# Optimization experiments

Hardware: AMD Instinct MI355X
Metric: run time of the kernel (lower is better)

Reference implementation:

```python
import jax, jax.numpy as jnp
import numpy as np

N = 100000      # nodes
D = 64          # raw node feature dim
E = 3200000     # edges
G = 128         # graphs in batch
RANK = 50
OVER = 10       # randomized-SVD oversampling
NPOW = 4        # subspace (power) iterations
ALPHA = 0.85    # pagerank alpha
HID = 32
NCLS = 696
F = 21 * D      # concat of [x] + 4 hop-1 + 16 hop-2 propagated tensors


def setup_inputs() -> dict:
    key = jax.random.key(0)
    ks = jax.random.split(key, 8)
    x = jax.random.normal(ks[0], (N, D), jnp.float32)
    rows = jax.random.randint(ks[1], (E,), 0, N, jnp.int32)
    cols = jax.random.randint(ks[2], (E,), 0, N, jnp.int32)
    graph_ids = jnp.sort(jax.random.randint(ks[3], (N,), 0, G, jnp.int32))
    w = jax.random.normal(ks[4], (F, 64), jnp.float32) / np.float32(np.sqrt(F))
    W1 = jax.random.normal(ks[5], (64, HID), jnp.float32) / np.float32(8.0)
    b1 = jnp.zeros((HID,), jnp.float32)
    W2 = jax.random.normal(ks[6], (HID, NCLS), jnp.float32) / np.float32(np.sqrt(HID))
    return dict(x=x, rows=rows, cols=cols, graph_ids=graph_ids, num_graphs=G,
                w=w, W1=W1, b1=b1, W2=W2)


def _prop_ops(X, rows, cols, deg, n):
    """Apply the 4 sparse operators to X. A[r,c]=1 per edge (rows[k], cols[k])."""
    ax = jax.ops.segment_sum(X[cols], rows, num_segments=n)          # A @ X
    t = ax / jnp.where(deg > 0, deg, 1.0)[:, None]                   # D^{-1} A @ X (transition)
    pr = ALPHA * t + ((1.0 - ALPHA) / n) * ax                        # pagerank-style operator
    dw = ax / (deg + 1e-5)[:, None]                                  # deepwalk: diag(1/(deg+eps)) A
    return [ax, t, pr, dw]


def _propagated(x, rows, cols):
    n = x.shape[0]
    deg = jax.ops.segment_sum(jnp.ones(rows.shape, x.dtype), rows, num_segments=n)
    h1 = _prop_ops(x, rows, cols, deg, n)                            # 4 tensors, hop 1
    h2 = [t2 for t1 in h1 for t2 in _prop_ops(t1, rows, cols, deg, n)]  # 16 tensors, hop 2
    return jnp.concatenate([x] + h1 + h2, axis=-1)                   # [n, 21*D]


def _rsvd(h, rank, key):
    """Deterministic randomized SVD (Halko et al.), QR-stabilized power iterations."""
    k = rank + OVER
    omega = jax.random.normal(key, (h.shape[1], k), h.dtype)
    Q = jnp.linalg.qr(h @ omega)[0]                                  # [n, k]
    for _ in range(NPOW):
        Q = jnp.linalg.qr(h.T @ Q)[0]
        Q = jnp.linalg.qr(h @ Q)[0]
    B = Q.T @ h                                                      # [k, F]
    ub, s, vt = jnp.linalg.svd(B, full_matrices=False)
    return (Q @ ub)[:, :rank], s[:rank], vt[:rank]


def reference(x, rows, cols, graph_ids, num_graphs, w, W1, b1, W2):
    h = _propagated(x, rows, cols)                                   # [n, F]
    u, s, vt = _rsvd(h, RANK, jax.random.key(42))
    us = u * s                                                       # [n, rank]
    term = us @ (vt @ w)                                             # [n, 64]
    hid = jax.nn.leaky_relu(term @ W1 + b1)                          # Dense + leaky_relu
    out_nodes = hid @ W2                                             # [n, num_classes]
    # pooling_adj.T.normalize_right(): each node belongs to exactly one graph,
    # so the column sums are 1 and this is a per-graph segment sum.
    return jax.ops.segment_sum(out_nodes, graph_ids, num_segments=num_graphs)
```

## Files before the change

### kernel.cpp

```cpp
#include <hip/hip_runtime.h>

#define NN   100000
#define DD   64
#define EE   3200000
#define GG   128
#define FF   1344
#define KK   60
#define RK   50
#define HIDN 32
#define NCL  696
#define BSPLIT 96
#define GSL  64
#define PN   40


typedef short short8 __attribute__((ext_vector_type(8)));
typedef float f32x4 __attribute__((ext_vector_type(4)));

__device__ __forceinline__ unsigned short f2bf(float x){
  unsigned u = __float_as_uint(x);
  unsigned r = u + 0x7fffu + ((u>>16)&1u);
  return (unsigned short)(r>>16);
}
__device__ __forceinline__ float bf2f(unsigned short h){
  return __uint_as_float(((unsigned)h)<<16);
}

__device__ __forceinline__ unsigned rotl32(unsigned x, unsigned r){ return (x<<r)|(x>>(32u-r)); }

__device__ __forceinline__ void threefry(unsigned& x0, unsigned& x1){
  const unsigned ks0 = 0u, ks1 = 42u, ks2 = 0x1BD11BDAu ^ 0u ^ 42u;
  unsigned ks[3] = {ks0, ks1, ks2};
  const unsigned rotA[4] = {13u,15u,26u,6u};
  const unsigned rotB[4] = {17u,29u,16u,24u};
  x0 += ks0; x1 += ks1;
  #pragma unroll
  for (int i = 0; i < 5; ++i){
    #pragma unroll
    for (int j = 0; j < 4; ++j){
      unsigned r = (i & 1) ? rotB[j] : rotA[j];
      x0 += x1; x1 = rotl32(x1, r); x1 ^= x0;
    }
    x0 += ks[(i+1)%3]; x1 += ks[(i+2)%3] + (unsigned)(i+1);
  }
}

__device__ __forceinline__ float bits_to_normal(unsigned bits){
  unsigned mant = bits >> 9;
  float f; { unsigned fb = 0x3f800000u | mant; f = __uint_as_float(fb); }
  f -= 1.0f;
  const float lo = -0.99999994f;
  float u = fmaf(f, 2.0f, lo);
  u = fmaxf(lo, u);
  float w = -log1pf(-u*u);
  float p;
  if (w < 5.0f){
    w -= 2.5f;
    p = 2.81022636e-08f;
    p = fmaf(p, w, 3.43273939e-07f);
    p = fmaf(p, w, -3.5233877e-06f);
    p = fmaf(p, w, -4.39150654e-06f);
    p = fmaf(p, w, 0.00021858087f);
    p = fmaf(p, w, -0.00125372503f);
    p = fmaf(p, w, -0.00417768164f);
    p = fmaf(p, w, 0.246640727f);
    p = fmaf(p, w, 1.50140941f);
  } else {
    w = sqrtf(w) - 3.0f;
    p = -0.000200214257f;
    p = fmaf(p, w, 0.000100950558f);
    p = fmaf(p, w, 0.00134934322f);
    p = fmaf(p, w, -0.00367342844f);
    p = fmaf(p, w, 0.00573950773f);
    p = fmaf(p, w, -0.0076224613f);
    p = fmaf(p, w, 0.00943887047f);
    p = fmaf(p, w, 1.00167406f);
    p = fmaf(p, w, 2.83297682f);
  }
  return 1.41421356f * (p * u);
}

__global__ void k_omega(float* __restrict__ om){
  int i = blockIdx.x*blockDim.x + threadIdx.x;
  if (i >= FF*KK) return;
  unsigned x0 = 0u, x1 = (unsigned)i;
  threefry(x0, x1);
  om[i] = bits_to_normal(x0 ^ x1);
}

__global__ void k_count(const int* __restrict__ rows, int* __restrict__ cnt){
  int e = blockIdx.x*blockDim.x + threadIdx.x;
  if (e < EE) atomicAdd(&cnt[rows[e]], 1);
}

__global__ __launch_bounds__(1024) void k_scan1(const int* __restrict__ cnt,
    int* __restrict__ incl, int* __restrict__ bsums){
  __shared__ int buf[1024];
  int i = blockIdx.x*1024 + threadIdx.x;
  int v = (i < NN) ? cnt[i] : 0;
  buf[threadIdx.x] = v; __syncthreads();
  for (int ofs = 1; ofs < 1024; ofs <<= 1){
    int add = (threadIdx.x >= (unsigned)ofs) ? buf[threadIdx.x - ofs] : 0;
    __syncthreads();
    buf[threadIdx.x] += add;
    __syncthreads();
  }
  if (i < NN) incl[i] = buf[threadIdx.x];
  if (threadIdx.x == 1023) bsums[blockIdx.x] = buf[1023];
}

__global__ void k_scan2(int* __restrict__ bsums, int nb){
  if (threadIdx.x == 0){
    int run = 0;
    for (int i = 0; i < nb; ++i){ int v = bsums[i]; bsums[i] = run; run += v; }
  }
}

__global__ void k_scan3(const int* __restrict__ cnt, const int* __restrict__ bsums,
                        int* __restrict__ rowptr){
  int i = blockIdx.x*blockDim.x + threadIdx.x;
  if (i >= NN) return;
  int incl = rowptr[i];
  int ex = incl - cnt[i] + bsums[i >> 10];
  rowptr[i] = ex;
  if (i == NN-1) rowptr[NN] = ex + cnt[i];
}

__global__ void k_scatter(const int* __restrict__ rows, const int* __restrict__ cols,
                          const int* __restrict__ rowptr, int* __restrict__ tmpc,
                          int* __restrict__ csr){
  int e = blockIdx.x*blockDim.x + threadIdx.x;
  if (e >= EE) return;
  int r = rows[e];
  int p = atomicAdd(&tmpc[r], 1);
  csr[rowptr[r] + p] = cols[e];
}

__global__ void k_degr(const int* __restrict__ cnt, float* __restrict__ r1, float* __restrict__ r2){
  int i = blockIdx.x*blockDim.x + threadIdx.x;
  if (i >= NN) return;
  int d = cnt[i];
  float fd = (float)d;
  r1[i] = (d > 0) ? 1.0f/fd : 1.0f;
  r2[i] = 1.0f/(fd + 1e-5f);
}

__global__ void k_xcvt(const float* __restrict__ x,
                       unsigned short* __restrict__ xh, unsigned short* __restrict__ xl){
  int gid = blockIdx.x*blockDim.x + threadIdx.x;
  if (gid >= NN*64) return;
  float v = x[gid];
  unsigned short h = f2bf(v);
  xh[gid] = h;
  xl[gid] = f2bf(v - bf2f(h));
}

__global__ __launch_bounds__(256) void k_hop1(const float* __restrict__ x,
    const int* __restrict__ rp, const int* __restrict__ cc, float* __restrict__ ax,
    unsigned short* __restrict__ axh, unsigned short* __restrict__ axl){
  int n = blockIdx.x*4 + (threadIdx.x >> 6);
  int lane = threadIdx.x & 63;
  if (n >= NN) return;
  int s = rp[n], e = rp[n+1];
  float acc = 0.f;
  int idx = s;
  for (; idx + 8 <= e; idx += 8){
    int c0 = cc[idx], c1 = cc[idx+1], c2 = cc[idx+2], c3 = cc[idx+3];
    int c4 = cc[idx+4], c5 = cc[idx+5], c6 = cc[idx+6], c7 = cc[idx+7];
    float v0 = x[(size_t)c0*64 + lane];
    float v1 = x[(size_t)c1*64 + lane];
    float v2 = x[(size_t)c2*64 + lane];
    float v3 = x[(size_t)c3*64 + lane];
    float v4 = x[(size_t)c4*64 + lane];
    float v5 = x[(size_t)c5*64 + lane];
    float v6 = x[(size_t)c6*64 + lane];
    float v7 = x[(size_t)c7*64 + lane];
    acc += ((v0 + v1) + (v2 + v3)) + ((v4 + v5) + (v6 + v7));
  }
  for (; idx < e; ++idx) acc += x[(size_t)cc[idx]*64 + lane];
  size_t o = (size_t)n*64 + lane;
  ax[o] = acc;
  unsigned short h = f2bf(acc);
  axh[o] = h;
  axl[o] = f2bf(acc - bf2f(h));
}

__global__ __launch_bounds__(256) void k_hop2(const int* __restrict__ rp, const int* __restrict__ cc,
    const float* __restrict__ ax, const float* __restrict__ r1, const float* __restrict__ r2,
    unsigned short* __restrict__ s0h, unsigned short* __restrict__ s0l,
    unsigned short* __restrict__ s1h, unsigned short* __restrict__ s1l,
    unsigned short* __restrict__ s3h, unsigned short* __restrict__ s3l){
  int n = blockIdx.x*4 + (threadIdx.x >> 6);
  int lane = threadIdx.x & 63;
  if (n >= NN) return;
  int s = rp[n], e = rp[n+1];
  float v_s0 = 0.f, v_s1 = 0.f, v_s3 = 0.f;
  int idx = s;
  for (; idx + 8 <= e; idx += 8){
    int c0 = cc[idx], c1 = cc[idx+1], c2 = cc[idx+2], c3 = cc[idx+3];
    int c4 = cc[idx+4], c5 = cc[idx+5], c6 = cc[idx+6], c7 = cc[idx+7];
    float v0 = ax[(size_t)c0*64 + lane], a0 = r1[c0], b0 = r2[c0];
    float v1 = ax[(size_t)c1*64 + lane], a1 = r1[c1], b1 = r2[c1];
    float v2 = ax[(size_t)c2*64 + lane], a2 = r1[c2], b2 = r2[c2];
    float v3 = ax[(size_t)c3*64 + lane], a3 = r1[c3], b3 = r2[c3];
    float v4 = ax[(size_t)c4*64 + lane], a4 = r1[c4], b4 = r2[c4];
    float v5 = ax[(size_t)c5*64 + lane], a5 = r1[c5], b5 = r2[c5];
    float v6 = ax[(size_t)c6*64 + lane], a6 = r1[c6], b6 = r2[c6];
    float v7 = ax[(size_t)c7*64 + lane], a7 = r1[c7], b7 = r2[c7];
    v_s0 += ((v0 + v1) + (v2 + v3)) + ((v4 + v5) + (v6 + v7));
    v_s1 = fmaf(v0,a0,fmaf(v1,a1,fmaf(v2,a2,fmaf(v3,a3,v_s1))));
    v_s1 = fmaf(v4,a4,fmaf(v5,a5,fmaf(v6,a6,fmaf(v7,a7,v_s1))));
    v_s3 = fmaf(v0,b0,fmaf(v1,b1,fmaf(v2,b2,fmaf(v3,b3,v_s3))));
    v_s3 = fmaf(v4,b4,fmaf(v5,b5,fmaf(v6,b6,fmaf(v7,b7,v_s3))));
  }
  for (; idx < e; ++idx){
    int c = cc[idx];
    float v = ax[(size_t)c*64 + lane];
    v_s0 += v;
    v_s1 = fmaf(v, r1[c], v_s1);
    v_s3 = fmaf(v, r2[c], v_s3);
  }
  size_t o = (size_t)n*64 + lane;
  unsigned short h0 = f2bf(v_s0);
  s0h[o] = h0; s0l[o] = f2bf(v_s0 - bf2f(h0));
  unsigned short h1 = f2bf(v_s1);
  s1h[o] = h1; s1l[o] = f2bf(v_s1 - bf2f(h1));
  unsigned short h3 = f2bf(v_s3);
  s3h[o] = h3; s3l[o] = f2bf(v_s3 - bf2f(h3));
}

__global__ void k_beff(const float* __restrict__ B,
                       unsigned short* __restrict__ Beh, unsigned short* __restrict__ Bel){
  int gid = blockIdx.x*blockDim.x + threadIdx.x;
  if (gid >= 20*4096) return;
  int p = gid >> 12;
  int rem = gid & 4095;
  int c = rem >> 6, r = rem & 63;
  int t = p >> 2, j = p & 3;
  float val = 0.f;
  if (c < KK){
    if (t == 0)      val = (j == 0) ? B[(0*64 + r)*60 + c] : 0.f;
    else if (t == 1) val = B[((1+j)*64 + r)*60 + c];
    else if (t == 2) val = B[((5+j)*64 + r)*60 + c] + 1.5e-6f*B[((13+j)*64 + r)*60 + c];
    else if (t == 3) val = B[((9+j)*64 + r)*60 + c] + 0.85f  *B[((13+j)*64 + r)*60 + c];
    else             val = B[((17+j)*64 + r)*60 + c];
  }
  unsigned short h = f2bf(val);
  Beh[gid] = h;
  Bel[gid] = f2bf(val - bf2f(h));
}

__global__ __launch_bounds__(256) void k_beffT(const float* __restrict__ Z,
    const float* __restrict__ Rtot,
    unsigned short* __restrict__ Beh, unsigned short* __restrict__ Bel){
  __shared__ float Br[64][61];
  __shared__ float Rt[60][64];
  int p = blockIdx.x;
  int t2 = p >> 2, j = p & 3;
  int tid = threadIdx.x;
  if (t2 == 0 && j != 0){
    for (int o = tid; o < 4096; o += 256){ Beh[(size_t)p*4096 + o] = 0; Bel[(size_t)p*4096 + o] = 0; }
    return;
  }
  for (int i = tid; i < 3840; i += 256){
    int r = i >> 6, c = i & 63;
    if (c < 60) Rt[r][c] = Rtot[r*60 + c];
  }
  for (int o = tid; o < 64*60; o += 256){
    int r = o / 60, k = o - (o/60)*60;
    float v;
    if (t2 == 0)      v = Z[(0*64 + r)*60 + k];
    else if (t2 == 1) v = Z[((1+j)*64 + r)*60 + k];
    else if (t2 == 2) v = Z[((5+j)*64 + r)*60 + k] + 1.5e-6f*Z[((13+j)*64 + r)*60 + k];
    else if (t2 == 3) v = Z[((9+j)*64 + r)*60 + k] + 0.85f  *Z[((13+j)*64 + r)*60 + k];
    else              v = Z[((17+j)*64 + r)*60 + k];
    Br[r][k] = v;
  }
  __syncthreads();
  for (int o = tid; o < 4096; o += 256){
    int c = o >> 6, r = o & 63;
    float s = 0.f;
    if (c < KK){
      #pragma unroll 10
      for (int kp = 0; kp < 60; ++kp) s = fmaf(Br[r][kp], Rt[kp][c], s);
    }
    unsigned short h = f2bf(s);
    Beh[(size_t)p*4096 + o] = h;
    Bel[(size_t)p*4096 + o] = f2bf(s - bf2f(h));
  }
}

__global__ __launch_bounds__(256) void k_qcvt(const float* __restrict__ Q,
    const float* __restrict__ r1, const float* __restrict__ r2,
    unsigned short* __restrict__ Qjh, unsigned short* __restrict__ Qjl){
  __shared__ float Qs[64][65];
  __shared__ float c1s[64], c3s[64];
  int n0 = blockIdx.x*64;
  int tid = threadIdx.x;
  for (int i = tid; i < 64*60; i += 256){
    int nl = i/60, k = i - (i/60)*60;
    int gn = n0 + nl;
    Qs[nl][k] = (gn < NN) ? Q[(size_t)gn*KK + k] : 0.f;
  }
  if (tid < 64){
    int gn = n0 + tid;
    c1s[tid] = (gn < NN) ? r1[gn] : 0.f;
    c3s[tid] = (gn < NN) ? r2[gn] : 0.f;
  }
  __syncthreads();
  for (int o = tid; o < 3*64*64; o += 256){
    int nl = o & 63;
    int jk = o >> 6;
    int gn = n0 + nl;
    if (gn >= NN) continue;
    int j = jk >> 6, k = jk & 63;
    float v = (k < KK) ? Qs[nl][k] : 0.f;
    float c = (j == 0) ? 1.f : ((j == 1) ? c1s[nl] : c3s[nl]);
    float sv = c * v;
    unsigned short h = f2bf(sv);
    Qjh[(size_t)jk*NN + gn] = h;
    Qjl[(size_t)jk*NN + gn] = f2bf(sv - bf2f(h));
  }
}

__device__ __forceinline__ void fma44(const float4 a, const float4 b, float (&acc)[4][4]){
  acc[0][0] = fmaf(a.x,b.x,acc[0][0]); acc[0][1] = fmaf(a.x,b.y,acc[0][1]);
  acc[0][2] = fmaf(a.x,b.z,acc[0][2]); acc[0][3] = fmaf(a.x,b.w,acc[0][3]);
  acc[1][0] = fmaf(a.y,b.x,acc[1][0]); acc[1][1] = fmaf(a.y,b.y,acc[1][1]);
  acc[1][2] = fmaf(a.y,b.z,acc[1][2]); acc[1][3] = fmaf(a.y,b.w,acc[1][3]);
  acc[2][0] = fmaf(a.z,b.x,acc[2][0]); acc[2][1] = fmaf(a.z,b.y,acc[2][1]);
  acc[2][2] = fmaf(a.z,b.z,acc[2][2]); acc[2][3] = fmaf(a.z,b.w,acc[2][3]);
  acc[3][0] = fmaf(a.w,b.x,acc[3][0]); acc[3][1] = fmaf(a.w,b.y,acc[3][1]);
  acc[3][2] = fmaf(a.w,b.z,acc[3][2]); acc[3][3] = fmaf(a.w,b.w,acc[3][3]);
}

__global__ __launch_bounds__(256) void k_fwd(
    const unsigned short* __restrict__ xh, const unsigned short* __restrict__ xl,
    const unsigned short* __restrict__ axh, const unsigned short* __restrict__ axl,
    const unsigned short* __restrict__ s0h, const unsigned short* __restrict__ s0l,
    const unsigned short* __restrict__ s1h, const unsigned short* __restrict__ s1l,
    const unsigned short* __restrict__ s3h, const unsigned short* __restrict__ s3l,
    const unsigned short* __restrict__ Beh, const unsigned short* __restrict__ Bel,
    const float* __restrict__ r1, const float* __restrict__ r2,
    float* __restrict__ Y, float* __restrict__ Cpart){
  __shared__ __align__(16) unsigned short AB[4*64*72];
  __shared__ float cS[4][64];
  unsigned short* Ah = AB;
  unsigned short* Al = AB + 64*72;
  unsigned short* Bh = AB + 2*64*72;
  unsigned short* Bl = AB + 3*64*72;
  float* As2 = (float*)AB;
  const unsigned short* Tsh[5] = {xh, axh, s0h, s1h, s3h};
  const unsigned short* Tsl[5] = {xl, axl, s0l, s1l, s3l};
  int n0 = blockIdx.x*64;
  int tid = threadIdx.x;
  int lane = tid & 63, wid = tid >> 6;
  int rowb = (wid & 1)*32, colb = (wid >> 1)*32;
  int l15 = lane & 15, l4 = lane >> 4;

  if (tid < 64){
    int gn = n0 + tid;
    float r1v = 0.f, r2v = 0.f, one = 0.f;
    if (gn < NN){ r1v = r1[gn]; r2v = r2[gn]; one = 1.f; }
    cS[0][tid] = one;
    cS[1][tid] = r1v;
    cS[2][tid] = fmaf(0.85f, r1v, 1.5e-6f*one);
    cS[3][tid] = r2v;
  }

  f32x4 master[2][2] = {};
  int curt = -1;
  for (int plin = 0; plin < 17; ++plin){
    int t  = (plin == 0) ? 0 : (((plin-1) >> 2) + 1);
    int jj = (plin == 0) ? 0 : ((plin-1) & 3);
    int p  = (plin == 0) ? 0 : (plin + 3);
    if (t != curt){
      __syncthreads();
      const unsigned short* Th = Tsh[t];
      const unsigned short* Tl = Tsl[t];
      #pragma unroll
      for (int l = 0; l < 2; ++l){
        int li = tid + l*256;
        int n = li >> 3, f8 = (li & 7)*8;
        int gn = n0 + n;
        uint4 hv = make_uint4(0,0,0,0), lv = make_uint4(0,0,0,0);
        if (gn < NN){
          hv = *(const uint4*)(Th + (size_t)gn*64 + f8);
          lv = *(const uint4*)(Tl + (size_t)gn*64 + f8);
        }
        *(uint4*)(Ah + n*72 + f8) = hv;
        *(uint4*)(Al + n*72 + f8) = lv;
      }
      curt = t;
    }
    __syncthreads();
    #pragma unroll
    for (int l = 0; l < 2; ++l){
      int li = tid + l*256;
      int c = li >> 3, k8 = (li & 7)*8;
      uint4 hv = *(const uint4*)(Beh + (size_t)p*4096 + c*64 + k8);
      uint4 lv = *(const uint4*)(Bel + (size_t)p*4096 + c*64 + k8);
      *(uint4*)(Bh + c*72 + k8) = hv;
      *(uint4*)(Bl + c*72 + k8) = lv;
    }
    __syncthreads();

    float cvv[2][4];
    #pragma unroll
    for (int rg = 0; rg < 2; ++rg)
      #pragma unroll
      for (int r = 0; r < 4; ++r)
        cvv[rg][r] = cS[jj][rowb + rg*16 + l4*4 + r];

    f32x4 part[2][2] = {};
    #pragma unroll
    for (int s = 0; s < 2; ++s){
      int kc = s*32 + l4*8;
      short8 a0h = *(const short8*)(Ah + (rowb      + l15)*72 + kc);
      short8 a1h = *(const short8*)(Ah + (rowb + 16 + l15)*72 + kc);
      short8 a0l = *(const short8*)(Al + (rowb      + l15)*72 + kc);
      short8 a1l = *(const short8*)(Al + (rowb + 16 + l15)*72 + kc);
      #pragma unroll
      for (int cg = 0; cg < 2; ++cg){
        short8 bh = *(const short8*)(Bh + (colb + cg*16 + l15)*72 + kc);
        short8 bl = *(const short8*)(Bl + (colb + cg*16 + l15)*72 + kc);
        part[0][cg] = __builtin_amdgcn_mfma_f32_16x16x32_bf16(a0h, bh, part[0][cg], 0, 0, 0);
        part[0][cg] = __builtin_amdgcn_mfma_f32_16x16x32_bf16(a0h, bl, part[0][cg], 0, 0, 0);
        part[0][cg] = __builtin_amdgcn_mfma_f32_16x16x32_bf16(a0l, bh, part[0][cg], 0, 0, 0);
        part[1][cg] = __builtin_amdgcn_mfma_f32_16x16x32_bf16(a1h, bh, part[1][cg], 0, 0, 0);
        part[1][cg] = __builtin_amdgcn_mfma_f32_16x16x32_bf16(a1h, bl, part[1][cg], 0, 0, 0);
        part[1][cg] = __builtin_amdgcn_mfma_f32_16x16x32_bf16(a1l, bh, part[1][cg], 0, 0, 0);
      }
    }
    #pragma unroll
    for (int rg = 0; rg < 2; ++rg)
      #pragma unroll
      for (int cg = 0; cg < 2; ++cg)
        #pragma unroll
        for (int r = 0; r < 4; ++r)
          master[rg][cg][r] = fmaf(cvv[rg][r], part[rg][cg][r], master[rg][cg][r]);
  }

  #pragma unroll
  for (int rg = 0; rg < 2; ++rg)
    #pragma unroll
    for (int cg = 0; cg < 2; ++cg)
      #pragma unroll
      for (int r = 0; r < 4; ++r){
        int n = rowb + rg*16 + l4*4 + r;
        int c = colb + cg*16 + l15;
        int gn = n0 + n;
        if (gn < NN && c < KK) Y[(size_t)gn*KK + c] = master[rg][cg][r];
      }

  __syncthreads();
  #pragma unroll
  for (int rg = 0; rg < 2; ++rg)
    #pragma unroll
    for (int cg = 0; cg < 2; ++cg)
      #pragma unroll
      for (int r = 0; r < 4; ++r){
        int n = rowb + rg*16 + l4*4 + r;
        int c = colb + cg*16 + l15;
        As2[n*68 + c] = master[rg][cg][r];
      }
  __syncthreads();
  {
    int tx = tid & 15, ty = tid >> 4;
    float g[4][4] = {};
    #pragma unroll 4
    for (int n = 0; n < 64; ++n){
      float4 a = *(const float4*)(As2 + n*68 + tx*4);
      float4 b = *(const float4*)(As2 + n*68 + ty*4);
      fma44(a, b, g);
    }
    float* slab = Cpart + (size_t)(blockIdx.x & (GSL-1))*3600;
    #pragma unroll
    for (int i = 0; i < 4; ++i){
      int r = tx*4 + i;
      #pragma unroll
      for (int j = 0; j < 4; ++j){
        int c = ty*4 + j;
        if (r < KK && c < KK) atomicAdd(&slab[r*KK + c], g[i][j]);
      }
    }
  }
}

__global__ __launch_bounds__(256) void k_bwd(
    const unsigned short* __restrict__ xh, const unsigned short* __restrict__ xl,
    const unsigned short* __restrict__ axh, const unsigned short* __restrict__ axl,
    const unsigned short* __restrict__ s0h, const unsigned short* __restrict__ s0l,
    const unsigned short* __restrict__ s1h, const unsigned short* __restrict__ s1l,
    const unsigned short* __restrict__ s3h, const unsigned short* __restrict__ s3l,
    const unsigned short* __restrict__ Qjh, const unsigned short* __restrict__ Qjl,
    float* __restrict__ Ppart){
  const unsigned short* Th = (blockIdx.x==0)?xh:(blockIdx.x==1)?axh:(blockIdx.x==2)?s0h:(blockIdx.x==3)?s1h:s3h;
  const unsigned short* Tl = (blockIdx.x==0)?xl:(blockIdx.x==1)?axl:(blockIdx.x==2)?s0l:(blockIdx.x==3)?s1l:s3l;
  const int TT = (NN + 31)/32;
  int per = (TT + BSPLIT - 1)/BSPLIT;
  int t0 = blockIdx.y * per;
  int t1 = t0 + per; if (t1 > TT) t1 = TT;

  __shared__ __align__(16) unsigned short Ah[64*PN];
  __shared__ __align__(16) unsigned short Al[64*PN];
  __shared__ __align__(16) unsigned short Bh3[3*64*PN];
  __shared__ __align__(16) unsigned short Bl3[3*64*PN];

  int tid = threadIdx.x;
  int lane = tid & 63, wid = tid >> 6;
  int rowb = (wid & 1)*32, colb = (wid >> 1)*32;
  int l15 = lane & 15, l4 = lane >> 4;

  f32x4 master[3][2][2] = {};

  for (int tl = t0; tl < t1; ++tl){
    int nb = tl*32;
    __syncthreads();
    {
      int n = tid >> 3, f8 = (tid & 7)*8;
      int gn = nb + n;
      uint4 hv = make_uint4(0,0,0,0), lv = make_uint4(0,0,0,0);
      if (gn < NN){
        hv = *(const uint4*)(Th + (size_t)gn*64 + f8);
        lv = *(const uint4*)(Tl + (size_t)gn*64 + f8);
      }
      const unsigned short* hp = (const unsigned short*)&hv;
      const unsigned short* lp = (const unsigned short*)&lv;
      #pragma unroll
      for (int i = 0; i < 8; ++i){
        Ah[(f8+i)*PN + n] = hp[i];
        Al[(f8+i)*PN + n] = lp[i];
      }
    }
    #pragma unroll
    for (int u = 0; u < 3; ++u){
      int l = tid + u*256;
      int row = l >> 2, ch = (l & 3)*8;
      uint4 hv = *(const uint4*)(Qjh + (size_t)row*NN + nb + ch);
      uint4 lv = *(const uint4*)(Qjl + (size_t)row*NN + nb + ch);
      *(uint4*)(Bh3 + row*PN + ch) = hv;
      *(uint4*)(Bl3 + row*PN + ch) = lv;
    }
    __syncthreads();
    short8 a0h = *(const short8*)(Ah + (rowb      + l15)*PN + l4*8);
    short8 a1h = *(const short8*)(Ah + (rowb + 16 + l15)*PN + l4*8);
    short8 a0l = *(const short8*)(Al + (rowb      + l15)*PN + l4*8);
    short8 a1l = *(const short8*)(Al + (rowb + 16 + l15)*PN + l4*8);
    #pragma unroll
    for (int jj = 0; jj < 3; ++jj){
      #pragma unroll
      for (int cg = 0; cg < 2; ++cg){
        short8 bh = *(const short8*)(Bh3 + jj*64*PN + (colb + cg*16 + l15)*PN + l4*8);
        short8 bl = *(const short8*)(Bl3 + jj*64*PN + (colb + cg*16 + l15)*PN + l4*8);
        master[jj][0][cg] = __builtin_amdgcn_mfma_f32_16x16x32_bf16(a0h, bh, master[jj][0][cg], 0, 0, 0);
        master[jj][0][cg] = __builtin_amdgcn_mfma_f32_16x16x32_bf16(a0h, bl, master[jj][0][cg], 0, 0, 0);
        master[jj][0][cg] = __builtin_amdgcn_mfma_f32_16x16x32_bf16(a0l, bh, master[jj][0][cg], 0, 0, 0);
        master[jj][1][cg] = __builtin_amdgcn_mfma_f32_16x16x32_bf16(a1h, bh, master[jj][1][cg], 0, 0, 0);
        master[jj][1][cg] = __builtin_amdgcn_mfma_f32_16x16x32_bf16(a1h, bl, master[jj][1][cg], 0, 0, 0);
        master[jj][1][cg] = __builtin_amdgcn_mfma_f32_16x16x32_bf16(a1l, bh, master[jj][1][cg], 0, 0, 0);
      }
    }
  }

  float* dst = Ppart + (size_t)blockIdx.y * 76800;
  #pragma unroll
  for (int jj = 0; jj < 3; ++jj){
    int j = (jj == 2) ? 3 : jj;
    #pragma unroll
    for (int rg = 0; rg < 2; ++rg)
      #pragma unroll
      for (int cg = 0; cg < 2; ++cg)
        #pragma unroll
        for (int r = 0; r < 4; ++r){
          int f = rowb + rg*16 + l4*4 + r;
          int kcol = colb + cg*16 + l15;
          if (kcol < KK)
            dst[(size_t)((blockIdx.x*4 + j)*64 + f)*60 + kcol] = master[jj][rg][cg][r];
        }
  }
}

__global__ void k_zasm(const float* __restrict__ Ppart, float* __restrict__ Z){
  int gid = blockIdx.x*blockDim.x + threadIdx.x;
  if (gid >= FF*KK) return;
  int f = gid / 60, k = gid - (gid/60)*60;
  int b = f >> 6, fi = f & 63;
  auto raw = [&](int t, int j)->float{
    size_t e = (size_t)((t*4 + j)*64 + fi)*60 + k;
    float s = 0.f;
    for (int bb = 0; bb < BSPLIT; ++bb) s += Ppart[(size_t)bb*76800 + e];
    return s;
  };
  auto fetch = [&](int t, int j)->float{
    if (j == 2) return 0.85f*raw(t,1) + 1.5e-6f*raw(t,0);
    return raw(t,j);
  };
  float val;
  if (b == 0)      val = raw(0,0);
  else if (b < 5)  val = fetch(1, b-1);
  else if (b < 9)  val = fetch(2, b-5);
  else if (b < 13) val = fetch(3, b-9);
  else if (b < 17) val = 0.85f*fetch(3, b-13) + 1.5e-6f*fetch(2, b-13);
  else             val = fetch(4, b-17);
  Z[gid] = val;
}

__global__ __launch_bounds__(256) void k_syrkp(const float* __restrict__ X, int nrows,
                                               float* __restrict__ Cpart){
  const int TTs = (nrows + 15)/16;
  int per = (TTs + gridDim.x - 1)/gridDim.x;
  int t0 = blockIdx.x*per;
  int t1 = t0 + per; if (t1 > TTs) t1 = TTs;
  __shared__ float Xs[16][64];
  int tid = threadIdx.x;
  int tx = tid & 15, ty = tid >> 4;
  float acc[4][4] = {};
  for (int tl = t0; tl < t1; ++tl){
    int nbase = tl*16;
    if (tid < 240){
      int n = tid / 15, ci = tid - (tid/15)*15;
      float4 v = make_float4(0.f,0.f,0.f,0.f);
      int gn = nbase + n;
      if (gn < nrows) v = *(const float4*)(X + (size_t)gn*KK + ci*4);
      *(float4*)&Xs[n][ci*4] = v;
    } else {
      int n = tid - 240;
      Xs[n][60]=0.f; Xs[n][61]=0.f; Xs[n][62]=0.f; Xs[n][63]=0.f;
    }
    __syncthreads();
    #pragma unroll
    for (int n = 0; n < 16; ++n){
      float4 a = *(const float4*)&Xs[n][tx*4];
      float4 b = *(const float4*)&Xs[n][ty*4];
      fma44(a, b, acc);
    }
    __syncthreads();
  }
  float* dst = Cpart + (size_t)blockIdx.x*3600;
  #pragma unroll
  for (int i = 0; i < 4; ++i){
    int r = tx*4 + i;
    #pragma unroll
    for (int j = 0; j < 4; ++j){
      int c = ty*4 + j;
      if (r < KK && c < KK) dst[r*KK + c] = acc[i][j];
    }
  }
}

__global__ void k_cred(const float* __restrict__ Cpart, int nparts, float* __restrict__ Cm){
  int gid = blockIdx.x*blockDim.x + threadIdx.x;
  if (gid >= 3600) return;
  float s = 0.f;
  for (int b = 0; b < nparts; ++b) s += Cpart[(size_t)b*3600 + gid];
  Cm[gid] = s;
}

__global__ __launch_bounds__(256) void k_cholinv(const float* __restrict__ Cin,
                                                 float* __restrict__ Rinv){
  __shared__ float R[60][65];
  __shared__ float Ri[60][65];
  __shared__ float Tmp[30][33];
  __shared__ float ridge;
  int t = threadIdx.x;
  for (int i = t; i < 3840; i += 256){
    int r = i >> 6, c = i & 63;
    if (c < 60) R[r][c] = Cin[r*60 + c];
  }
  __syncthreads();
  if (t == 0){
    float tr = 0.f;
    for (int i = 0; i < 60; ++i) tr += R[i][i];
    ridge = 1e-7f*(tr/60.f) + 1e-30f;
  }
  __syncthreads();
  if (t < 60) R[t][t] += ridge;
  __syncthreads();
  for (int j = 0; j < 60; ++j){
    float d  = fmaxf(R[j][j], 1e-30f);
    float dp = (j > 0) ? fmaxf(R[j-1][j-1], 1e-30f) : 1.f;
    float inv = 1.0f / d;
    float rsp = (j > 0) ? (1.0f / sqrtf(dp)) : 1.f;
    int nrow = 59 - j;
    for (int task = t; task < (nrow+1)*64; task += 256){
      int rr = task >> 6, i2 = task & 63;
      if (rr < nrow){
        int k = j + 1 + rr;
        if (i2 >= k && i2 < 60) R[k][i2] -= R[j][k]*R[j][i2]*inv;
      } else {
        if (j > 0 && i2 >= j-1 && i2 < 60) R[j-1][i2] *= rsp;
      }
    }
    __syncthreads();
  }
  if (t == 0) R[59][59] = sqrtf(fmaxf(R[59][59], 1e-30f));
  __syncthreads();
  for (int i = t; i < 3840; i += 256){ int r = i >> 6, c = i & 63; Ri[r][c] = 0.f; }
  __syncthreads();
  if (t < 60){
    int c = t;
    int lo = (c < 30) ? 0 : 30;
    Ri[c][c] = 1.0f / R[c][c];
    for (int i = c-1; i >= lo; --i){
      float s = 0.f;
      for (int k = i+1; k <= c; ++k) s += R[i][k]*Ri[k][c];
      Ri[i][c] = -s / R[i][i];
    }
  }
  __syncthreads();
  for (int idx2 = t; idx2 < 960; idx2 += 256){
    int r = idx2 >> 5, c = idx2 & 31;
    if (c < 30){
      float s = 0.f;
      for (int k = 0; k <= c; ++k) s += R[r][30+k]*Ri[30+k][30+c];
      Tmp[r][c] = s;
    }
  }
  __syncthreads();
  for (int idx2 = t; idx2 < 960; idx2 += 256){
    int r = idx2 >> 5, c = idx2 & 31;
    if (c < 30){
      float s = 0.f;
      for (int k = r; k < 30; ++k) s += Ri[r][k]*Tmp[k][c];
      Ri[r][30+c] = -s;
    }
  }
  __syncthreads();
  for (int i = t; i < 3600; i += 256) Rinv[i] = Ri[i/60][i%60];
}

__global__ __launch_bounds__(256) void k_cholinv2(const float* __restrict__ Gin,
                                                  float* __restrict__ Rinv){
  __shared__ float G[60][65];
  __shared__ float RN[60][65];
  __shared__ float T1[60][65];
  __shared__ float G2[60][65];
  __shared__ float Tmp[30][33];
  __shared__ float ridge;
  int t = threadIdx.x;
  for (int i = t; i < 3840; i += 256){
    int r = i >> 6, c = i & 63;
    if (c < 60){ G[r][c] = Gin[r*60 + c]; RN[r][c] = Rinv[r*60 + c]; }
  }
  __syncthreads();
  for (int o = t; o < 3600; o += 256){
    int i = o/60, j = o - (o/60)*60;
    float s = 0.f;
    for (int k = 0; k <= j; ++k) s = fmaf(G[i][k], RN[k][j], s);
    T1[i][j] = s;
  }
  __syncthreads();
  for (int o = t; o < 3600; o += 256){
    int i = o/60, j = o - (o/60)*60;
    float s = 0.f;
    for (int k = 0; k <= i; ++k) s = fmaf(RN[k][i], T1[k][j], s);
    G2[i][j] = s;
  }
  __syncthreads();
  if (t == 0){
    float tr = 0.f;
    for (int i = 0; i < 60; ++i) tr += G2[i][i];
    ridge = 1e-7f*(tr/60.f) + 1e-30f;
  }
  __syncthreads();
  if (t < 60) G2[t][t] += ridge;
  __syncthreads();
  for (int j = 0; j < 60; ++j){
    float d  = fmaxf(G2[j][j], 1e-30f);
    float dp = (j > 0) ? fmaxf(G2[j-1][j-1], 1e-30f) : 1.f;
    float inv = 1.0f / d;
    float rsp = (j > 0) ? (1.0f / sqrtf(dp)) : 1.f;
    int nrow = 59 - j;
    for (int task = t; task < (nrow+1)*64; task += 256){
      int rr = task >> 6, i2 = task & 63;
      if (rr < nrow){
        int k = j + 1 + rr;
        if (i2 >= k && i2 < 60) G2[k][i2] -= G2[j][k]*G2[j][i2]*inv;
      } else {
        if (j > 0 && i2 >= j-1 && i2 < 60) G2[j-1][i2] *= rsp;
      }
    }
    __syncthreads();
  }
  if (t == 0) G2[59][59] = sqrtf(fmaxf(G2[59][59], 1e-30f));
  __syncthreads();
  for (int i = t; i < 3840; i += 256){ int r = i >> 6, c = i & 63; T1[r][c] = 0.f; }
  __syncthreads();
  if (t < 60){
    int c = t;
    int lo = (c < 30) ? 0 : 30;
    T1[c][c] = 1.0f / G2[c][c];
    for (int i = c-1; i >= lo; --i){
      float s = 0.f;
      for (int k = i+1; k <= c; ++k) s += G2[i][k]*T1[k][c];
      T1[i][c] = -s / G2[i][i];
    }
  }
  __syncthreads();
  for (int idx2 = t; idx2 < 960; idx2 += 256){
    int r = idx2 >> 5, c = idx2 & 31;
    if (c < 30){
      float s = 0.f;
      for (int k = 0; k <= c; ++k) s += G2[r][30+k]*T1[30+k][30+c];
      Tmp[r][c] = s;
    }
  }
  __syncthreads();
  for (int idx2 = t; idx2 < 960; idx2 += 256){
    int r = idx2 >> 5, c = idx2 & 31;
    if (c < 30){
      float s = 0.f;
      for (int k = r; k < 30; ++k) s += T1[r][k]*Tmp[k][c];
      T1[r][30+c] = -s;
    }
  }
  __syncthreads();
  for (int o = t; o < 3600; o += 256){
    int i = o/60, j = o - (o/60)*60;
    float s = 0.f;
    if (i <= j){
      for (int k = i; k <= j; ++k) s = fmaf(RN[i][k], T1[k][j], s);
    }
    Rinv[o] = s;
  }
}

__global__ __launch_bounds__(256) void k_applyR(const float* Yin,
    const float* __restrict__ Rinv, float* Xout, int nrows){
  __shared__ float Rs[3600];
  for (int i = threadIdx.x; i < 3600; i += 256) Rs[i] = Rinv[i];
  __syncthreads();
  int w = threadIdx.x >> 6, lane = threadIdx.x & 63;
  #pragma unroll
  for (int r = 0; r < 4; ++r){
    int n = blockIdx.x*16 + w*4 + r;
    if (n >= nrows) continue;
    const float* y = Yin + (size_t)n*KK;
    float accv = 0.f;
    #pragma unroll 10
    for (int k2 = 0; k2 < KK; ++k2) accv = fmaf(y[k2], Rs[k2*KK + lane], accv);
    if (lane < KK) Xout[(size_t)n*KK + lane] = accv;
  }
}

__global__ void k_wb(const float* __restrict__ Z, const float* __restrict__ w,
                     float* __restrict__ WB){
  int gid = blockIdx.x*blockDim.x + threadIdx.x;
  if (gid >= KK*64) return;
  int r = gid >> 6, d = gid & 63;
  float acc = 0.f;
  for (int f = 0; f < FF; ++f) acc = fmaf(Z[(size_t)f*KK + r], w[(size_t)f*64 + d], acc);
  WB[gid] = acc;
}

__global__ __launch_bounds__(512) void k_jacobi(const float* __restrict__ Min,
                                                float* __restrict__ U50){
  __shared__ float A[60][65];
  __shared__ float Vv[60][65];
  __shared__ float cs[32], sn[32];
  __shared__ int pp[32], qq[32];
  __shared__ float ev[64];
  __shared__ int idx[64];
  int t = threadIdx.x;
  for (int i = t; i < 3840; i += 512){
    int r = i >> 6, c = i & 63;
    if (c < 60){ A[r][c] = Min[r*60 + c]; Vv[r][c] = (r == c) ? 1.f : 0.f; }
  }
  __syncthreads();
  for (int sweep = 0; sweep < 3; ++sweep){
    for (int round = 0; round < 59; ++round){
      if (t < 30){
        int i = t, j2 = 59 - t;
        int p = (i == 0) ? 0 : ((i - 1 + round) % 59 + 1);
        int q = ((j2 - 1 + round) % 59 + 1);
        if (p > q){ int tv = p; p = q; q = tv; }
        pp[t] = p; qq[t] = q;
        float app = A[p][p], aqq = A[q][q], apq = A[p][q];
        float c, s;
        if (fabsf(apq) < 1e-36f){ c = 1.f; s = 0.f; }
        else {
          float tau = (aqq - app) / (2.f * apq);
          float tt = ((tau >= 0.f) ? 1.f : -1.f) / (fabsf(tau) + sqrtf(1.f + tau*tau));
          c = 1.f / sqrtf(1.f + tt*tt);
          s = tt * c;
        }
        cs[t] = c; sn[t] = s;
      }
      __syncthreads();
      for (int task = t; task < 1920; task += 512){
        int k = task >> 6, i = task & 63;
        if (i < 60){
          int p = pp[k], q = qq[k];
          float c = cs[k], s = sn[k];
          float aip = A[i][p], aiq = A[i][q];
          A[i][p] = c*aip - s*aiq;  A[i][q] = s*aip + c*aiq;
          float vip = Vv[i][p], viq = Vv[i][q];
          Vv[i][p] = c*vip - s*viq; Vv[i][q] = s*vip + c*viq;
        }
      }
      __syncthreads();
      for (int task = t; task < 1920; task += 512){
        int k = task >> 6, i = task & 63;
        if (i < 60){
          int p = pp[k], q = qq[k];
          float c = cs[k], s = sn[k];
          float api = A[p][i], aqi = A[q][i];
          A[p][i] = c*api - s*aqi;  A[q][i] = s*api + c*aqi;
        }
      }
      __syncthreads();
    }
  }
  if (t < 60) ev[t] = A[t][t];
  __syncthreads();
  if (t < 60){
    float mine = ev[t];
    int rank = 0;
    for (int j = 0; j < 60; ++j){
      float o = ev[j];
      if (o > mine || (o == mine && j < t)) ++rank;
    }
    if (rank < RK) idx[rank] = t;
  }
  __syncthreads();
  for (int i2 = t; i2 < 60*RK; i2 += 512){
    int r = i2 / RK, c = i2 - (i2/RK)*RK;
    U50[i2] = Vv[r][idx[c]];
  }
}

__global__ __launch_bounds__(256) void k_chain(const float* __restrict__ U50,
    const float* __restrict__ WB, const float* __restrict__ W1, float* __restrict__ TW1){
  __shared__ float Us[60][52];
  __shared__ float WBs[60][64];
  __shared__ float G[50][64];
  __shared__ float Ts[60][64];
  int t = threadIdx.x;
  for (int i = t; i < 60*RK; i += 256) Us[i/RK][i%RK] = U50[i];
  for (int i = t; i < 3840; i += 256) WBs[i>>6][i&63] = WB[i];
  __syncthreads();
  for (int o = t; o < RK*64; o += 256){
    int r = o >> 6, d = o & 63;
    float acc = 0.f;
    #pragma unroll 10
    for (int i = 0; i < KK; ++i) acc = fmaf(Us[i][r], WBs[i][d], acc);
    G[r][d] = acc;
  }
  __syncthreads();
  for (int o = t; o < KK*64; o += 256){
    int i = o >> 6, d = o & 63;
    float acc = 0.f;
    #pragma unroll 10
    for (int r = 0; r < RK; ++r) acc = fmaf(Us[i][r], G[r][d], acc);
    Ts[i][d] = acc;
  }
  __syncthreads();
  for (int o = t; o < KK*HIDN; o += 256){
    int i = o >> 5, j = o & 31;
    float acc = 0.f;
    #pragma unroll 8
    for (int d = 0; d < 64; ++d) acc = fmaf(Ts[i][d], W1[d*HIDN + j], acc);
    TW1[o] = acc;
  }
}

__global__ __launch_bounds__(256) void k_hid(const float* __restrict__ Q,
    const float* __restrict__ TW1, const float* __restrict__ b1, float* __restrict__ hid){
  __shared__ float Ts[KK*HIDN];
  __shared__ float bs[HIDN];
  for (int i = threadIdx.x; i < KK*HIDN; i += 256) Ts[i] = TW1[i];
  if (threadIdx.x < HIDN) bs[threadIdx.x] = b1[threadIdx.x];
  __syncthreads();
  int gid = blockIdx.x*256 + threadIdx.x;
  if (gid >= NN*HIDN) return;
  int n = gid >> 5, j = gid & 31;
  const float* q = Q + (size_t)n*KK;
  float a = bs[j];
  #pragma unroll 10
  for (int k2 = 0; k2 < KK; ++k2) a = fmaf(q[k2], Ts[k2*HIDN + j], a);
  hid[gid] = (a >= 0.f) ? a : 0.01f*a;
}

__global__ void k_gstart(const int* __restrict__ gids, int* __restrict__ gst){
  int g = blockIdx.x*blockDim.x + threadIdx.x;
  if (g > GG) return;
  if (g == GG){ gst[GG] = NN; return; }
  int lo = 0, hi = NN;
  while (lo < hi){ int mid = (lo + hi) >> 1; if (gids[mid] < g) lo = mid + 1; else hi = mid; }
  gst[g] = lo;
}

__global__ __launch_bounds__(256) void k_gpool(const float* __restrict__ hid,
    const int* __restrict__ gst, float* __restrict__ pooled){
  int g = blockIdx.x;
  __shared__ float part[8][32];
  int w = threadIdx.x >> 5, lane = threadIdx.x & 31;
  int s = gst[g], e = gst[g+1];
  float acc = 0.f;
  for (int n = s + w; n < e; n += 8)
    acc += hid[(size_t)n*HIDN + lane];
  part[w][lane] = acc;
  __syncthreads();
  if (w == 0){
    float v = 0.f;
    #pragma unroll
    for (int i = 0; i < 8; ++i) v += part[i][lane];
    pooled[g*HIDN + lane] = v;
  }
}

__global__ void k_out(const float* __restrict__ pooled, const float* __restrict__ W2,
                      float* __restrict__ out){
  int gid = blockIdx.x*blockDim.x + threadIdx.x;
  if (gid >= GG*NCL) return;
  int g = gid / NCL, c = gid - (gid/NCL)*NCL;
  const float* p = pooled + g*HIDN;
  float acc = 0.f;
  #pragma unroll
  for (int k = 0; k < HIDN; ++k) acc = fmaf(p[k], W2[(size_t)k*NCL + c], acc);
  out[gid] = acc;
}

extern "C" void kernel_launch(void* const* d_in, const int* in_sizes, int n_in,
                              void* d_out, int out_size, void* d_ws, size_t ws_size,
                              hipStream_t stream){
  (void)in_sizes; (void)n_in; (void)out_size;
  const float* x   = (const float*)d_in[0];
  const int*  rows = (const int*)d_in[1];
  const int*  cols = (const int*)d_in[2];
  const int*  gids = (const int*)d_in[3];
  const float* wM  = (const float*)d_in[5];
  const float* W1  = (const float*)d_in[6];
  const float* b1  = (const float*)d_in[7];
  const float* W2  = (const float*)d_in[8];
  float* out = (float*)d_out;

  char* base = (char*)d_ws;
  size_t off = 0;
  auto alloc = [&](size_t bytes)->char*{
    off = (off + 255) & ~(size_t)255;
    char* p = base + off; off += bytes; return p;
  };
  float* ax    = (float*)alloc((size_t)NN*64*4);
  int*   csr   = (int*)  alloc((size_t)EE*4);
  unsigned short* Qjh = (unsigned short*)ax;
  unsigned short* xh  = (unsigned short*)alloc((size_t)NN*64*2);
  unsigned short* xl  = (unsigned short*)alloc((size_t)NN*64*2);
  unsigned short* axh = (unsigned short*)alloc((size_t)NN*64*2);
  unsigned short* axl = (unsigned short*)alloc((size_t)NN*64*2);
  unsigned short* s0h = (unsigned short*)alloc((size_t)NN*64*2);
  unsigned short* s0l = (unsigned short*)alloc((size_t)NN*64*2);
  unsigned short* s1h = (unsigned short*)alloc((size_t)NN*64*2);
  unsigned short* s1l = (unsigned short*)alloc((size_t)NN*64*2);
  unsigned short* s3h = (unsigned short*)alloc((size_t)NN*64*2);
  unsigned short* s3l = (unsigned short*)alloc((size_t)NN*64*2);
  float* Y     = (float*)alloc((size_t)NN*KK*4);
  unsigned short* Qjl = (unsigned short*)alloc((size_t)3*64*NN*2);
  float* Ppart = (float*)alloc((size_t)BSPLIT*76800*4);
  unsigned short* Beh = (unsigned short*)alloc((size_t)20*4096*2);
  unsigned short* Bel = (unsigned short*)alloc((size_t)20*4096*2);
  float* Om    = (float*)alloc((size_t)FF*KK*4);
  float* Zf    = (float*)alloc((size_t)FF*KK*4);
  float* Cm    = (float*)alloc(3600*4);
  float* Rinv  = (float*)alloc(3600*4);
  float* Mm    = (float*)alloc(3600*4);
  float* U50   = (float*)alloc(60*RK*4);
  float* WB    = (float*)alloc(KK*64*4);
  float* TW1   = (float*)alloc(KK*HIDN*4);
  float* pooled= (float*)alloc((size_t)GG*HIDN*4);
  float* r1    = (float*)alloc((size_t)NN*4);
  float* r2    = (float*)alloc((size_t)NN*4);
  int* cnt     = (int*)alloc((size_t)NN*4);
  int* rowptr  = (int*)alloc((size_t)(NN+1)*4);
  int* tmpc    = (int*)alloc((size_t)NN*4);
  int* gst     = (int*)alloc((size_t)(GG+1)*4);
  int* bsums   = (int*)alloc(256*4);
  float* hid   = (float*)Qjl;
  float* Cpart = Ppart;
  if (off > ws_size) return;

  const int SCAN_B = (NN + 1023) / 1024;

  hipMemsetAsync(cnt, 0, (size_t)NN*4, stream);
  k_count<<<(EE+255)/256, 256, 0, stream>>>(rows, cnt);
  k_scan1<<<SCAN_B, 1024, 0, stream>>>(cnt, rowptr, bsums);
  k_scan2<<<1, 64, 0, stream>>>(bsums, SCAN_B);
  k_scan3<<<(NN+255)/256, 256, 0, stream>>>(cnt, bsums, rowptr);
  hipMemsetAsync(tmpc, 0, (size_t)NN*4, stream);
  k_scatter<<<(EE+255)/256, 256, 0, stream>>>(rows, cols, rowptr, tmpc, csr);
  k_degr<<<(NN+255)/256, 256, 0, stream>>>(cnt, r1, r2);

  k_xcvt<<<(NN*64+255)/256, 256, 0, stream>>>(x, xh, xl);
  k_hop1<<<(NN+3)/4, 256, 0, stream>>>(x, rowptr, csr, ax, axh, axl);
  k_hop2<<<(NN+3)/4, 256, 0, stream>>>(rowptr, csr, ax, r1, r2, s0h, s0l, s1h, s1l, s3h, s3l);

  k_omega<<<(FF*KK+255)/256, 256, 0, stream>>>(Om);

  auto fwdg = [&](){
    hipMemsetAsync(Cpart, 0, (size_t)GSL*3600*4, stream);
    k_fwd<<<(NN+63)/64, 256, 0, stream>>>(xh, xl, axh, axl, s0h, s0l, s1h, s1l, s3h, s3l,
                                          Beh, Bel, r1, r2, Y, Cpart);
  };
  auto bwd = [&](const float* Qbuf){
    k_qcvt<<<(NN+63)/64, 256, 0, stream>>>(Qbuf, r1, r2, Qjh, Qjl);
    k_bwd<<<dim3(5, BSPLIT), 256, 0, stream>>>(xh, xl, axh, axl, s0h, s0l, s1h, s1l, s3h, s3l,
                                               Qjh, Qjl, Ppart);
    k_zasm<<<(FF*KK+255)/256, 256, 0, stream>>>(Ppart, Zf);
  };

  k_beff<<<(20*4096+255)/256, 256, 0, stream>>>(Om, Beh, Bel);
  fwdg();

  for (int it = 0; it < 4; ++it){
    k_cred<<<15, 256, 0, stream>>>(Cpart, GSL, Cm);
    k_cholinv<<<1, 256, 0, stream>>>(Cm, Rinv);
    bwd(Y);
    k_syrkp<<<84, 256, 0, stream>>>(Zf, FF, Cpart);
    k_cred<<<15, 256, 0, stream>>>(Cpart, 84, Cm);
    k_cholinv2<<<1, 256, 0, stream>>>(Cm, Rinv);
    k_beffT<<<20, 256, 0, stream>>>(Zf, Rinv, Beh, Bel);
    fwdg();
  }

  k_cred<<<15, 256, 0, stream>>>(Cpart, GSL, Cm);
  k_cholinv<<<1, 256, 0, stream>>>(Cm, Rinv);
  k_applyR<<<(NN+15)/16, 256, 0, stream>>>(Y, Rinv, Y, NN);

  bwd(Y);
  k_syrkp<<<84, 256, 0, stream>>>(Zf, FF, Cpart);
  k_cred<<<15, 256, 0, stream>>>(Cpart, 84, Mm);
  k_wb<<<(KK*64+255)/256, 256, 0, stream>>>(Zf, wM, WB);

  k_jacobi<<<1, 512, 0, stream>>>(Mm, U50);
  k_chain<<<1, 256, 0, stream>>>(U50, WB, W1, TW1);

  k_hid<<<(NN*HIDN+255)/256, 256, 0, stream>>>(Y, TW1, b1, hid);
  k_gstart<<<1, 256, 0, stream>>>(gids, gst);
  k_gpool<<<GG, 256, 0, stream>>>(hid, gst, pooled);
  k_out<<<(GG*NCL+255)/256, 256, 0, stream>>>(pooled, W2, out);
}
```

Measured before the change: 4.033 ms.

## Pre-transpose propagated tensors for backward GEMM and fold final R into small matrices

Adds a one-time transpose kernel that writes the five bf16 hi/lo propagated tensors in feature-major layout, so the backward h^T Q GEMM can load A tiles with contiguous vector loads instead of scattered shared-memory transposes on every call. It also stops applying the final R^-1 to the full N×60 Y matrix. R^-1 is applied to the small F×60 Zf instead, and folded into the TW1 chain matrix. This saves a full pass over Y but needs extra workspace for the transposed copies, with a fallback path when that workspace is not available.

Measured after the change: 3.975 ms. About the same (-1.4%).

```diff
diff --git a/kernel.cpp b/kernel.cpp
--- a/kernel.cpp
+++ b/kernel.cpp
@@ -229,6 +229,49 @@
   s3h[o] = h3; s3l[o] = f2bf(v_s3 - bf2f(h3));
 }
 
+__global__ __launch_bounds__(256) void k_tcvt(
+    const unsigned short* __restrict__ xh, const unsigned short* __restrict__ xl,
+    const unsigned short* __restrict__ axh, const unsigned short* __restrict__ axl,
+    const unsigned short* __restrict__ s0h, const unsigned short* __restrict__ s0l,
+    const unsigned short* __restrict__ s1h, const unsigned short* __restrict__ s1l,
+    const unsigned short* __restrict__ s3h, const unsigned short* __restrict__ s3l,
+    unsigned short* __restrict__ TTh, unsigned short* __restrict__ TTl){
+  __shared__ unsigned short Sh[64][72];
+  __shared__ unsigned short Sl[64][72];
+  int t = blockIdx.y;
+  const unsigned short* inh = (t==0)?xh:(t==1)?axh:(t==2)?s0h:(t==3)?s1h:s3h;
+  const unsigned short* inl = (t==0)?xl:(t==1)?axl:(t==2)?s0l:(t==3)?s1l:s3l;
+  int n0 = blockIdx.x*64;
+  int tid = threadIdx.x;
+  #pragma unroll
+  for (int l = 0; l < 2; ++l){
+    int li = tid + l*256;
+    int n = li >> 3, f8 = (li & 7)*8;
+    int gn = n0 + n;
+    uint4 hv = make_uint4(0,0,0,0), lv = make_uint4(0,0,0,0);
+    if (gn < NN){
+      hv = *(const uint4*)(inh + (size_t)gn*64 + f8);
+      lv = *(const uint4*)(inl + (size_t)gn*64 + f8);
+    }
+    *(uint4*)(&Sh[n][f8]) = hv;
+    *(uint4*)(&Sl[n][f8]) = lv;
+  }
+  __syncthreads();
+  #pragma unroll
+  for (int l = 0; l < 2; ++l){
+    int li = tid + l*256;
+    int f = li >> 3, ch = (li & 7)*8;
+    int gn0 = n0 + ch;
+    if (gn0 + 8 <= NN){
+      unsigned short hv[8], lv2[8];
+      #pragma unroll
+      for (int i = 0; i < 8; ++i){ hv[i] = Sh[ch+i][f]; lv2[i] = Sl[ch+i][f]; }
+      *(uint4*)(TTh + (size_t)(t*64+f)*NN + gn0) = *(uint4*)hv;
+      *(uint4*)(TTl + (size_t)(t*64+f)*NN + gn0) = *(uint4*)lv2;
+    }
+  }
+}
+
 __global__ void k_beff(const float* __restrict__ B,
                        unsigned short* __restrict__ Beh, unsigned short* __restrict__ Bel){
   int gid = blockIdx.x*blockDim.x + threadIdx.x;
@@ -497,10 +540,10 @@
     float* __restrict__ Ppart){
   const unsigned short* Th = (blockIdx.x==0)?xh:(blockIdx.x==1)?axh:(blockIdx.x==2)?s0h:(blockIdx.x==3)?s1h:s3h;
   const unsigned short* Tl = (blockIdx.x==0)?xl:(blockIdx.x==1)?axl:(blockIdx.x==2)?s0l:(blockIdx.x==3)?s1l:s3l;
-  const int TT = (NN + 31)/32;
-  int per = (TT + BSPLIT - 1)/BSPLIT;
+  const int TT2 = (NN + 31)/32;
+  int per = (TT2 + BSPLIT - 1)/BSPLIT;
   int t0 = blockIdx.y * per;
-  int t1 = t0 + per; if (t1 > TT) t1 = TT;
+  int t1 = t0 + per; if (t1 > TT2) t1 = TT2;
 
   __shared__ __align__(16) unsigned short Ah[64*PN];
   __shared__ __align__(16) unsigned short Al[64*PN];
@@ -532,6 +575,86 @@
         Ah[(f8+i)*PN + n] = hp[i];
         Al[(f8+i)*PN + n] = lp[i];
       }
+    }
+    #pragma unroll
+    for (int u = 0; u < 3; ++u){
+      int l = tid + u*256;
+      int row = l >> 2, ch = (l & 3)*8;
+      uint4 hv = *(const uint4*)(Qjh + (size_t)row*NN + nb + ch);
+      uint4 lv = *(const uint4*)(Qjl + (size_t)row*NN + nb + ch);
+      *(uint4*)(Bh3 + row*PN + ch) = hv;
+      *(uint4*)(Bl3 + row*PN + ch) = lv;
+    }
+    __syncthreads();
+    short8 a0h = *(const short8*)(Ah + (rowb      + l15)*PN + l4*8);
+    short8 a1h = *(const short8*)(Ah + (rowb + 16 + l15)*PN + l4*8);
+    short8 a0l = *(const short8*)(Al + (rowb      + l15)*PN + l4*8);
+    short8 a1l = *(const short8*)(Al + (rowb + 16 + l15)*PN + l4*8);
+    #pragma unroll
+    for (int jj = 0; jj < 3; ++jj){
+      #pragma unroll
+      for (int cg = 0; cg < 2; ++cg){
+        short8 bh = *(const short8*)(Bh3 + jj*64*PN + (colb + cg*16 + l15)*PN + l4*8);
+        short8 bl = *(const short8*)(Bl3 + jj*64*PN + (colb + cg*16 + l15)*PN + l4*8);
+        master[jj][0][cg] = __builtin_amdgcn_mfma_f32_16x16x32_bf16(a0h, bh, master[jj][0][cg], 0, 0, 0);
+        master[jj][0][cg] = __builtin_amdgcn_mfma_f32_16x16x32_bf16(a0h, bl, master[jj][0][cg], 0, 0, 0);
+        master[jj][0][cg] = __builtin_amdgcn_mfma_f32_16x16x32_bf16(a0l, bh, master[jj][0][cg], 0, 0, 0);
+        master[jj][1][cg] = __builtin_amdgcn_mfma_f32_16x16x32_bf16(a1h, bh, master[jj][1][cg], 0, 0, 0);
+        master[jj][1][cg] = __builtin_amdgcn_mfma_f32_16x16x32_bf16(a1h, bl, master[jj][1][cg], 0, 0, 0);
+        master[jj][1][cg] = __builtin_amdgcn_mfma_f32_16x16x32_bf16(a1l, bh, master[jj][1][cg], 0, 0, 0);
+      }
+    }
+  }
+
+  float* dst = Ppart + (size_t)blockIdx.y * 76800;
+  #pragma unroll
+  for (int jj = 0; jj < 3; ++jj){
+    int j = (jj == 2) ? 3 : jj;
+    #pragma unroll
+    for (int rg = 0; rg < 2; ++rg)
+      #pragma unroll
+      for (int cg = 0; cg < 2; ++cg)
+        #pragma unroll
+        for (int r = 0; r < 4; ++r){
+          int f = rowb + rg*16 + l4*4 + r;
+          int kcol = colb + cg*16 + l15;
+          if (kcol < KK)
+            dst[(size_t)((blockIdx.x*4 + j)*64 + f)*60 + kcol] = master[jj][rg][cg][r];
+        }
+  }
+}
+
+__global__ __launch_bounds__(256) void k_bwd_T(
+    const unsigned short* __restrict__ TTh, const unsigned short* __restrict__ TTl,
+    const unsigned short* __restrict__ Qjh, const unsigned short* __restrict__ Qjl,
+    float* __restrict__ Ppart){
+  int tb = blockIdx.x;
+  const int TT2 = (NN + 31)/32;
+  int per = (TT2 + BSPLIT - 1)/BSPLIT;
+  int t0 = blockIdx.y * per;
+  int t1 = t0 + per; if (t1 > TT2) t1 = TT2;
+
+  __shared__ __align__(16) unsigned short Ah[64*PN];
+  __shared__ __align__(16) unsigned short Al[64*PN];
+  __shared__ __align__(16) unsigned short Bh3[3*64*PN];
+  __shared__ __align__(16) unsigned short Bl3[3*64*PN];
+
+  int tid = threadIdx.x;
+  int lane = tid & 63, wid = tid >> 6;
+  int rowb = (wid & 1)*32, colb = (wid >> 1)*32;
+  int l15 = lane & 15, l4 = lane >> 4;
+
+  f32x4 master[3][2][2] = {};
+
+  for (int tl = t0; tl < t1; ++tl){
+    int nb = tl*32;
+    __syncthreads();
+    {
+      int f = tid >> 2, ch = (tid & 3)*8;
+      uint4 hv = *(const uint4*)(TTh + (size_t)(tb*64+f)*NN + nb + ch);
+      uint4 lv = *(const uint4*)(TTl + (size_t)(tb*64+f)*NN + nb + ch);
+      *(uint4*)(Ah + f*PN + ch) = hv;
+      *(uint4*)(Al + f*PN + ch) = lv;
     }
     #pragma unroll
     for (int u = 0; u < 3; ++u){
@@ -931,11 +1054,13 @@
 }
 
 __global__ __launch_bounds__(256) void k_chain(const float* __restrict__ U50,
-    const float* __restrict__ WB, const float* __restrict__ W1, float* __restrict__ TW1){
+    const float* __restrict__ WB, const float* __restrict__ W1,
+    const float* __restrict__ Rinv, float* __restrict__ TW1){
   __shared__ float Us[60][52];
   __shared__ float WBs[60][64];
   __shared__ float G[50][64];
   __shared__ float Ts[60][64];
+  __shared__ float Tm2[60][33];
   int t = threadIdx.x;
   for (int i = t; i < 60*RK; i += 256) Us[i/RK][i%RK] = U50[i];
   for (int i = t; i < 3840; i += 256) WBs[i>>6][i&63] = WB[i];
@@ -961,6 +1086,13 @@
     float acc = 0.f;
     #pragma unroll 8
     for (int d = 0; d < 64; ++d) acc = fmaf(Ts[i][d], W1[d*HIDN + j], acc);
+    Tm2[i][j] = acc;
+  }
+  __syncthreads();
+  for (int o = t; o < KK*HIDN; o += 256){
+    int i = o >> 5, j = o & 31;
+    float acc = 0.f;
+    for (int k = i; k < KK; ++k) acc = fmaf(Rinv[i*KK + k], Tm2[k][j], acc);
     TW1[o] = acc;
   }
 }
@@ -1078,7 +1210,11 @@
   int* bsums   = (int*)alloc(256*4);
   float* hid   = (float*)Qjl;
   float* Cpart = Ppart;
-  if (off > ws_size) return;
+  size_t off_base = off;
+  unsigned short* TTh = (unsigned short*)alloc((size_t)5*64*NN*2);
+  unsigned short* TTl = (unsigned short*)alloc((size_t)5*64*NN*2);
+  bool useTT = (off <= ws_size);
+  if (off_base > ws_size) return;
 
   const int SCAN_B = (NN + 1023) / 1024;
 
@@ -1094,6 +1230,9 @@
   k_xcvt<<<(NN*64+255)/256, 256, 0, stream>>>(x, xh, xl);
   k_hop1<<<(NN+3)/4, 256, 0, stream>>>(x, rowptr, csr, ax, axh, axl);
   k_hop2<<<(NN+3)/4, 256, 0, stream>>>(rowptr, csr, ax, r1, r2, s0h, s0l, s1h, s1l, s3h, s3l);
+  if (useTT)
+    k_tcvt<<<dim3((NN+63)/64, 5), 256, 0, stream>>>(xh, xl, axh, axl, s0h, s0l,
+                                                    s1h, s1l, s3h, s3l, TTh, TTl);
 
   k_omega<<<(FF*KK+255)/256, 256, 0, stream>>>(Om);
 
@@ -1104,8 +1243,11 @@
   };
   auto bwd = [&](const float* Qbuf){
     k_qcvt<<<(NN+63)/64, 256, 0, stream>>>(Qbuf, r1, r2, Qjh, Qjl);
-    k_bwd<<<dim3(5, BSPLIT), 256, 0, stream>>>(xh, xl, axh, axl, s0h, s0l, s1h, s1l, s3h, s3l,
-                                               Qjh, Qjl, Ppart);
+    if (useTT)
+      k_bwd_T<<<dim3(5, BSPLIT), 256, 0, stream>>>(TTh, TTl, Qjh, Qjl, Ppart);
+    else
+      k_bwd<<<dim3(5, BSPLIT), 256, 0, stream>>>(xh, xl, axh, axl, s0h, s0l, s1h, s1l,
+                                                 s3h, s3l, Qjh, Qjl, Ppart);
     k_zasm<<<(FF*KK+255)/256, 256, 0, stream>>>(Ppart, Zf);
   };
 
@@ -1125,15 +1267,14 @@
 
   k_cred<<<15, 256, 0, stream>>>(Cpart, GSL, Cm);
   k_cholinv<<<1, 256, 0, stream>>>(Cm, Rinv);
-  k_applyR<<<(NN+15)/16, 256, 0, stream>>>(Y, Rinv, Y, NN);
-
   bwd(Y);
+  k_applyR<<<(FF+15)/16, 256, 0, stream>>>(Zf, Rinv, Zf, FF);
   k_syrkp<<<84, 256, 0, stream>>>(Zf, FF, Cpart);
   k_cred<<<15, 256, 0, stream>>>(Cpart, 84, Mm);
   k_wb<<<(KK*64+255)/256, 256, 0, stream>>>(Zf, wM, WB);
 
   k_jacobi<<<1, 512, 0, stream>>>(Mm, U50);
-  k_chain<<<1, 256, 0, stream>>>(U50, WB, W1, TW1);
+  k_chain<<<1, 256, 0, stream>>>(U50, WB, W1, Rinv, TW1);
 
   k_hid<<<(NN*HIDN+255)/256, 256, 0, stream>>>(Y, TW1, b1, hid);
   k_gstart<<<1, 256, 0, stream>>>(gids, gst);
```
